# Performance work log

Hardware: AMD Instinct MI355X
Metric: run time of the kernel (lower is better)

The kernel has to match this reference:

```python
import jax, jax.numpy as jnp
import numpy as np

D_MODEL = 4096
HIDDEN = int(8 * D_MODEL / 3)  # 10922, as in the torch __init__
QMAX = 127.0

def fake_quant(t):
    """Symmetric per-tensor int8 fake-quantization (quantize -> dequantize).
    Emulates the quantize/dequantize boundaries of nn.quantized.Linear."""
    s = jnp.maximum(jnp.max(jnp.abs(t)) / QMAX, 1e-8)
    return jnp.clip(jnp.round(t / s), -QMAX, QMAX) * s

def setup_inputs() -> dict:
    key = jax.random.key(0)
    kx, kg, ku, kd, kbg, kbu, kbd = jax.random.split(key, 7)
    x = jax.random.normal(kx, (4096, D_MODEL), dtype=jnp.float32)
    # int8 weights stored dequantized in fp32 (scale * int8 grid applied in fake_quant)
    std = 1.0 / np.sqrt(D_MODEL)
    wg = jax.random.normal(kg, (HIDDEN, D_MODEL), dtype=jnp.float32) * std
    wu = jax.random.normal(ku, (HIDDEN, D_MODEL), dtype=jnp.float32) * std
    wd = jax.random.normal(kd, (D_MODEL, HIDDEN), dtype=jnp.float32) * (1.0 / np.sqrt(HIDDEN))
    bg = jax.random.normal(kbg, (HIDDEN,), dtype=jnp.float32) * 0.01
    bu = jax.random.normal(kbu, (HIDDEN,), dtype=jnp.float32) * 0.01
    bd = jax.random.normal(kbd, (D_MODEL,), dtype=jnp.float32) * 0.01
    return {"x": x, "wg": wg, "wu": wu, "wd": wd, "bg": bg, "bu": bu, "bd": bd}

def reference(x, wg, wu, wd, bg, bu, bd):
    # int8 quantized SwiGLU expert: each nn.quantized.Linear quantizes its
    # input, uses int8 weights, and emits a (re)quantized output.
    xq = fake_quant(x)
    gate = fake_quant(jnp.einsum('td,hd->th', xq, fake_quant(wg)) + bg)
    up = fake_quant(jnp.einsum('td,hd->th', xq, fake_quant(wu)) + bu)
    act = fake_quant(jax.nn.silu(gate) * up)  # SwiGLU, requantized at down_proj input
    out = jnp.einsum('th,dh->td', act, fake_quant(wd)) + bd
    return out
```

## Files before the change

kernel.cpp:

```cpp
#include <hip/hip_runtime.h>

#define D_MODEL 4096
#define HID     10922
#define HIDP    11008
#define MTOK    4096
#define QMAXF   127.0f

typedef _Float16 half8  __attribute__((ext_vector_type(8)));
typedef _Float16 half4v __attribute__((ext_vector_type(4)));
typedef float    floatx4 __attribute__((ext_vector_type(4)));

__device__ __forceinline__ void gl_lds16(const void* g, void* l) {
  __builtin_amdgcn_global_load_lds((__attribute__((address_space(1))) void*)g,
                                   (__attribute__((address_space(3))) void*)l,
                                   16, 0, 0);
}

__device__ __forceinline__ float slot_scale(const unsigned* slots, int idx) {
  return fmaxf(__uint_as_float(slots[idx]) / QMAXF, 1e-8f);
}

__global__ void absmax_k(const float* __restrict__ in, int n4, unsigned* __restrict__ slot) {
  int tid = blockIdx.x * blockDim.x + threadIdx.x;
  int stride = gridDim.x * blockDim.x;
  float m = 0.f;
  const float4* in4 = (const float4*)in;
  for (int i = tid; i < n4; i += stride) {
    float4 v = in4[i];
    m = fmaxf(m, fmaxf(fmaxf(fabsf(v.x), fabsf(v.y)), fmaxf(fabsf(v.z), fabsf(v.w))));
  }
  #pragma unroll
  for (int off = 32; off; off >>= 1) m = fmaxf(m, __shfl_down(m, off));
  __shared__ float sm[4];
  int lane = threadIdx.x & 63, w = threadIdx.x >> 6;
  if (!lane) sm[w] = m;
  __syncthreads();
  if (!threadIdx.x) {
    m = fmaxf(fmaxf(sm[0], sm[1]), fmaxf(sm[2], sm[3]));
    atomicMax(slot, __float_as_uint(m));
  }
}

__global__ void quant_k(const float* __restrict__ in, _Float16* __restrict__ out,
                        int rows_in, int cols_in, int cols_out, int total8,
                        const unsigned* __restrict__ slot) {
  float s = fmaxf(__uint_as_float(*slot) / QMAXF, 1e-8f);
  int t = blockIdx.x * blockDim.x + threadIdx.x;
  if (t >= total8) return;
  int idx = t * 8;
  int r = idx / cols_out;
  int c = idx - r * cols_out;
  half8 h;
  if (r < rows_in && c + 8 <= cols_in) {
    const float2* p = (const float2*)(in + (size_t)r * cols_in + c);
    #pragma unroll
    for (int j = 0; j < 4; ++j) {
      float2 v = p[j];
      float q0 = fminf(fmaxf(rintf(v.x / s), -QMAXF), QMAXF);
      float q1 = fminf(fmaxf(rintf(v.y / s), -QMAXF), QMAXF);
      h[2 * j]     = (_Float16)q0;
      h[2 * j + 1] = (_Float16)q1;
    }
  } else {
    #pragma unroll
    for (int j = 0; j < 8; ++j) {
      int cc = c + j;
      float v = 0.f;
      if (r < rows_in && cc < cols_in) v = in[(size_t)r * cols_in + cc];
      float q = fminf(fmaxf(rintf(v / s), -QMAXF), QMAXF);
      h[j] = (_Float16)q;
    }
  }
  *(half8*)(out + idx) = h;
}

__device__ __forceinline__ float act_val(float g, float u, float sg, float su) {
  float gq = fminf(fmaxf(rintf(g / sg), -QMAXF), QMAXF) * sg;
  float uq = fminf(fmaxf(rintf(u / su), -QMAXF), QMAXF) * su;
  float sig = (gq >= 0.f) ? (1.f / (1.f + expf(-gq)))
                          : (expf(gq) / (1.f + expf(gq)));
  return (gq * sig) * uq;
}

__global__ void act_max_k(const float* __restrict__ gate, const float* __restrict__ up,
                          const unsigned* __restrict__ slots, unsigned* __restrict__ outslot,
                          int n4) {
  float sg = slot_scale(slots, 4);
  float su = slot_scale(slots, 5);
  int tid = blockIdx.x * blockDim.x + threadIdx.x;
  int stride = gridDim.x * blockDim.x;
  float m = 0.f;
  const float4* g4 = (const float4*)gate;
  const float4* u4 = (const float4*)up;
  for (int i = tid; i < n4; i += stride) {
    float4 g = g4[i], u = u4[i];
    m = fmaxf(m, fabsf(act_val(g.x, u.x, sg, su)));
    m = fmaxf(m, fabsf(act_val(g.y, u.y, sg, su)));
    m = fmaxf(m, fabsf(act_val(g.z, u.z, sg, su)));
    m = fmaxf(m, fabsf(act_val(g.w, u.w, sg, su)));
  }
  #pragma unroll
  for (int off = 32; off; off >>= 1) m = fmaxf(m, __shfl_down(m, off));
  __shared__ float sm[4];
  int lane = threadIdx.x & 63, w = threadIdx.x >> 6;
  if (!lane) sm[w] = m;
  __syncthreads();
  if (!threadIdx.x) {
    m = fmaxf(fmaxf(sm[0], sm[1]), fmaxf(sm[2], sm[3]));
    atomicMax(outslot, __float_as_uint(m));
  }
}

__global__ void act_quant_k(const float* __restrict__ gate, const float* __restrict__ up,
                            const unsigned* __restrict__ slots, _Float16* __restrict__ actq,
                            int n4) {
  float sg = slot_scale(slots, 4);
  float su = slot_scale(slots, 5);
  float sa = slot_scale(slots, 6);
  int tid = blockIdx.x * blockDim.x + threadIdx.x;
  int stride = gridDim.x * blockDim.x;
  const float4* g4 = (const float4*)gate;
  const float4* u4 = (const float4*)up;
  for (int i = tid; i < n4; i += stride) {
    float4 g = g4[i], u = u4[i];
    float a0 = act_val(g.x, u.x, sg, su);
    float a1 = act_val(g.y, u.y, sg, su);
    float a2 = act_val(g.z, u.z, sg, su);
    float a3 = act_val(g.w, u.w, sg, su);
    half4v h;
    h[0] = (_Float16)fminf(fmaxf(rintf(a0 / sa), -QMAXF), QMAXF);
    h[1] = (_Float16)fminf(fmaxf(rintf(a1 / sa), -QMAXF), QMAXF);
    h[2] = (_Float16)fminf(fmaxf(rintf(a2 / sa), -QMAXF), QMAXF);
    h[3] = (_Float16)fminf(fmaxf(rintf(a3 / sa), -QMAXF), QMAXF);
    *(half4v*)(actq + (size_t)i * 4) = h;
  }
}

__global__ __launch_bounds__(256) void gemm_k(
    const _Float16* __restrict__ A, const _Float16* __restrict__ B,
    const float* __restrict__ bias, float* __restrict__ C,
    int K, int lda, int ldb, int ldc, int nbias,
    const unsigned* __restrict__ slots, int sa_idx, int sb_idx,
    unsigned* __restrict__ maxslot) {
  __shared__ __align__(16) _Float16 As[128 * 32];
  __shared__ __align__(16) _Float16 Bs[128 * 32];

  const int wave = threadIdx.x >> 6;
  const int lane = threadIdx.x & 63;
  const int wrow = wave >> 1, wcol = wave & 1;
  const int l16 = lane & 15, quad = lane >> 4;
  const int tm = blockIdx.x * 128, tn = blockIdx.y * 128;

  floatx4 acc[4][4] = {};

  const int so = wave * 2048 + lane * 16;
  const char* Ab = (const char*)A;
  const char* Bb = (const char*)B;

  for (int k0 = 0; k0 < K; k0 += 32) {
    #pragma unroll
    for (int p = 0; p < 2; ++p) {
      int bo = so + p * 1024;
      int row = bo >> 6;
      int csrc = ((bo >> 4) & 3) ^ ((row >> 1) & 3);
      gl_lds16(Ab + ((size_t)(tm + row) * lda + k0) * 2 + csrc * 16,
               (char*)As + wave * 2048 + p * 1024);
      gl_lds16(Bb + ((size_t)(tn + row) * ldb + k0) * 2 + csrc * 16,
               (char*)Bs + wave * 2048 + p * 1024);
    }
    __syncthreads();
    half8 af[4], bf[4];
    #pragma unroll
    for (int i = 0; i < 4; ++i) {
      int ra = wrow * 64 + i * 16 + l16;
      int rb = wcol * 64 + i * 16 + l16;
      af[i] = *(const half8*)((const char*)As + (ra * 64 + (quad ^ ((ra >> 1) & 3)) * 16));
      bf[i] = *(const half8*)((const char*)Bs + (rb * 64 + (quad ^ ((rb >> 1) & 3)) * 16));
    }
    #pragma unroll
    for (int i = 0; i < 4; ++i)
      #pragma unroll
      for (int j = 0; j < 4; ++j)
        acc[i][j] = __builtin_amdgcn_mfma_f32_16x16x32_f16(af[i], bf[j], acc[i][j], 0, 0, 0);
    __syncthreads();
  }

  float scale = slot_scale(slots, sa_idx) * slot_scale(slots, sb_idx);
  float mloc = 0.f;
  #pragma unroll
  for (int i = 0; i < 4; ++i) {
    int rg0 = tm + wrow * 64 + i * 16 + quad * 4;
    #pragma unroll
    for (int j = 0; j < 4; ++j) {
      int cg = tn + wcol * 64 + j * 16 + l16;
      float bv = (cg < nbias) ? bias[cg] : 0.f;
      #pragma unroll
      for (int r = 0; r < 4; ++r) {
        float v = acc[i][j][r] * scale + bv;
        C[(size_t)(rg0 + r) * ldc + cg] = v;
        mloc = fmaxf(mloc, fabsf(v));
      }
    }
  }
  #pragma unroll
  for (int off = 32; off; off >>= 1) mloc = fmaxf(mloc, __shfl_down(mloc, off));
  __shared__ float smx[4];
  if (!lane) smx[wave] = mloc;
  __syncthreads();
  if (!threadIdx.x)
    atomicMax(maxslot, __float_as_uint(fmaxf(fmaxf(smx[0], smx[1]), fmaxf(smx[2], smx[3]))));
}

extern "C" void kernel_launch(void* const* d_in, const int* in_sizes, int n_in,
                              void* d_out, int out_size, void* d_ws, size_t ws_size,
                              hipStream_t stream) {
  const float* x  = (const float*)d_in[0];
  const float* wg = (const float*)d_in[1];
  const float* wu = (const float*)d_in[2];
  const float* wd = (const float*)d_in[3];
  const float* bg = (const float*)d_in[4];
  const float* bu = (const float*)d_in[5];
  const float* bd = (const float*)d_in[6];
  float* out = (float*)d_out;

  char* ws = (char*)d_ws;
  unsigned* slots = (unsigned*)ws;
  const size_t XQ_B = (size_t)MTOK * D_MODEL * 2;
  const size_t WQ_B = (size_t)HIDP * D_MODEL * 2;
  const size_t GU_B = (size_t)MTOK * HIDP * 4;

  _Float16* xq   = (_Float16*)(ws + 256);
  _Float16* wgq  = (_Float16*)(ws + 256 + XQ_B);
  _Float16* wuq  = (_Float16*)(ws + 256 + XQ_B + WQ_B);
  float*    gate = (float*)   (ws + 256 + XQ_B + 2 * WQ_B);
  float*    up   = (float*)   (ws + 256 + XQ_B + 2 * WQ_B + GU_B);
  _Float16* actq = wgq;
  _Float16* wdq  = wuq;

  hipMemsetAsync(ws, 0, 256, stream);

  absmax_k<<<2048, 256, 0, stream>>>(x,  MTOK * D_MODEL / 4, slots + 0);
  absmax_k<<<2048, 256, 0, stream>>>(wg, HID * D_MODEL / 4,  slots + 1);
  absmax_k<<<2048, 256, 0, stream>>>(wu, HID * D_MODEL / 4,  slots + 2);
  absmax_k<<<2048, 256, 0, stream>>>(wd, MTOK * HID / 4,     slots + 3);

  {
    int t8 = MTOK * D_MODEL / 8;
    quant_k<<<(t8 + 255) / 256, 256, 0, stream>>>(x, xq, MTOK, D_MODEL, D_MODEL, t8, slots + 0);
    int w8 = HIDP * D_MODEL / 8;
    quant_k<<<(w8 + 255) / 256, 256, 0, stream>>>(wg, wgq, HID, D_MODEL, D_MODEL, w8, slots + 1);
    quant_k<<<(w8 + 255) / 256, 256, 0, stream>>>(wu, wuq, HID, D_MODEL, D_MODEL, w8, slots + 2);
  }

  {
    dim3 g1(MTOK / 128, HIDP / 128);
    gemm_k<<<g1, 256, 0, stream>>>(xq, wgq, bg, gate, D_MODEL, D_MODEL, D_MODEL, HIDP, HID,
                                   slots, 0, 1, slots + 4);
    gemm_k<<<g1, 256, 0, stream>>>(xq, wuq, bu, up,   D_MODEL, D_MODEL, D_MODEL, HIDP, HID,
                                   slots, 0, 2, slots + 5);
  }

  {
    int t8 = MTOK * HIDP / 8;
    quant_k<<<(t8 + 255) / 256, 256, 0, stream>>>(wd, wdq, MTOK, HID, HIDP, t8, slots + 3);
  }

  {
    int n4 = MTOK * HIDP / 4;
    act_max_k<<<4096, 256, 0, stream>>>(gate, up, slots, slots + 6, n4);
    act_quant_k<<<4096, 256, 0, stream>>>(gate, up, slots, actq, n4);
  }

  {
    dim3 g2(MTOK / 128, D_MODEL / 128);
    gemm_k<<<g2, 256, 0, stream>>>(actq, wdq, bd, out, HIDP, HIDP, HIDP, D_MODEL, D_MODEL,
                                   slots, 6, 3, slots + 7);
  }
}
```

Baseline: 2.490 ms.

## Rewrite GEMM as 256x256 tile with double-buffered LDS and phased MFMA pipeline

Replaces the 128x128, BK=32, 4-wave GEMM with a 256x256, BK=64, 8-wave kernel. Global-to-LDS loads are double-buffered and split into per-half stages, so each stage is issued inside one of eight compute phases. Explicit vmcnt waits, scheduling barriers and s_setprio raise around the MFMA bursts overlap memory traffic with matrix math and increase operand reuse per LDS byte. In exchange it uses about 128KB of LDS and large accumulator register state, which likely limits residency to one block per CU. The hand-managed wait counts are fragile.

```diff
diff --git a/kernel.cpp b/kernel.cpp
--- a/kernel.cpp
+++ b/kernel.cpp
@@ -136,63 +136,131 @@
   }
 }
 
-__global__ __launch_bounds__(256) void gemm_k(
+
+#define SBAR() do {                                                           \
+    __builtin_amdgcn_sched_barrier(0);                                        \
+    __builtin_amdgcn_s_barrier();                                             \
+    __builtin_amdgcn_sched_barrier(0);                                        \
+  } while (0)
+
+#define STAGE(GB, LS, LD, TB, KT, BUF, H) do {                                \
+    const char* _s = (GB) + ((size_t)((TB) + (H) * 128 + s_r0) * (LD)         \
+                             + (size_t)(KT) * 64) * 2 + s_cb;                 \
+    char* _d = (char*)(LS) + ((BUF) * 2 + (H)) * 16384 + wave * 1024;         \
+    gl_lds16(_s, _d);                                                         \
+    gl_lds16(_s + (size_t)(LD) * 128, _d + 8192);                             \
+  } while (0)
+
+#define PHASE(BUF, HM, HN, ...) do {                                          \
+    half8 af[4][2], bf[2][2];                                                 \
+    _Pragma("unroll")                                                         \
+    for (int i2 = 0; i2 < 4; ++i2) {                                          \
+      int gr = (HM) * 128 + wrow * 64 + i2 * 16 + l16;                        \
+      const char* pa = (const char*)As + ((BUF) * 2 + (gr >> 7)) * 16384      \
+                       + (gr & 127) * 128;                                    \
+      _Pragma("unroll")                                                       \
+      for (int ks = 0; ks < 2; ++ks)                                          \
+        af[i2][ks] = *(const half8*)(pa + (((ks * 4 + quad) ^ (l16 & 7)) * 16)); \
+    }                                                                         \
+    _Pragma("unroll")                                                         \
+    for (int j2 = 0; j2 < 2; ++j2) {                                          \
+      int gc = (HN) * 128 + wcol * 32 + j2 * 16 + l16;                        \
+      const char* pb = (const char*)Bs + ((BUF) * 2 + (gc >> 7)) * 16384      \
+                       + (gc & 127) * 128;                                    \
+      _Pragma("unroll")                                                       \
+      for (int ks = 0; ks < 2; ++ks)                                          \
+        bf[j2][ks] = *(const half8*)(pb + (((ks * 4 + quad) ^ (l16 & 7)) * 16)); \
+    }                                                                         \
+    __VA_ARGS__;                                                              \
+    SBAR();                                                                   \
+    __builtin_amdgcn_s_setprio(1);                                            \
+    _Pragma("unroll")                                                         \
+    for (int i2 = 0; i2 < 4; ++i2)                                            \
+      _Pragma("unroll")                                                       \
+      for (int j2 = 0; j2 < 2; ++j2)                                          \
+        _Pragma("unroll")                                                     \
+        for (int ks = 0; ks < 2; ++ks)                                        \
+          acc[(HM) * 4 + i2][(HN) * 2 + j2] =                                 \
+              __builtin_amdgcn_mfma_f32_16x16x32_f16(                         \
+                  af[i2][ks], bf[j2][ks],                                     \
+                  acc[(HM) * 4 + i2][(HN) * 2 + j2], 0, 0, 0);                \
+    __builtin_amdgcn_s_setprio(0);                                            \
+    SBAR();                                                                   \
+  } while (0)
+
+__global__ __launch_bounds__(512, 2) void gemm_k(
     const _Float16* __restrict__ A, const _Float16* __restrict__ B,
     const float* __restrict__ bias, float* __restrict__ C,
     int K, int lda, int ldb, int ldc, int nbias,
     const unsigned* __restrict__ slots, int sa_idx, int sb_idx,
     unsigned* __restrict__ maxslot) {
-  __shared__ __align__(16) _Float16 As[128 * 32];
-  __shared__ __align__(16) _Float16 Bs[128 * 32];
-
-  const int wave = threadIdx.x >> 6;
-  const int lane = threadIdx.x & 63;
-  const int wrow = wave >> 1, wcol = wave & 1;
+  __shared__ __align__(16) _Float16 As[2 * 2 * 128 * 64];
+  __shared__ __align__(16) _Float16 Bs[2 * 2 * 128 * 64];
+  __shared__ float smx[8];
+
+  const int tid = threadIdx.x;
+  const int wave = tid >> 6, lane = tid & 63;
+  const int wrow = wave >> 2, wcol = wave & 3;
   const int l16 = lane & 15, quad = lane >> 4;
-  const int tm = blockIdx.x * 128, tn = blockIdx.y * 128;
-
-  floatx4 acc[4][4] = {};
-
-  const int so = wave * 2048 + lane * 16;
+  const int tm = blockIdx.x * 256, tn = blockIdx.y * 256;
+
+  const int s_r0 = wave * 8 + (lane >> 3);
+  const int s_cb = ((lane & 7) ^ (lane >> 3)) * 16;
+
   const char* Ab = (const char*)A;
   const char* Bb = (const char*)B;
 
-  for (int k0 = 0; k0 < K; k0 += 32) {
-    #pragma unroll
-    for (int p = 0; p < 2; ++p) {
-      int bo = so + p * 1024;
-      int row = bo >> 6;
-      int csrc = ((bo >> 4) & 3) ^ ((row >> 1) & 3);
-      gl_lds16(Ab + ((size_t)(tm + row) * lda + k0) * 2 + csrc * 16,
-               (char*)As + wave * 2048 + p * 1024);
-      gl_lds16(Bb + ((size_t)(tn + row) * ldb + k0) * 2 + csrc * 16,
-               (char*)Bs + wave * 2048 + p * 1024);
-    }
-    __syncthreads();
-    half8 af[4], bf[4];
-    #pragma unroll
-    for (int i = 0; i < 4; ++i) {
-      int ra = wrow * 64 + i * 16 + l16;
-      int rb = wcol * 64 + i * 16 + l16;
-      af[i] = *(const half8*)((const char*)As + (ra * 64 + (quad ^ ((ra >> 1) & 3)) * 16));
-      bf[i] = *(const half8*)((const char*)Bs + (rb * 64 + (quad ^ ((rb >> 1) & 3)) * 16));
-    }
-    #pragma unroll
-    for (int i = 0; i < 4; ++i)
-      #pragma unroll
-      for (int j = 0; j < 4; ++j)
-        acc[i][j] = __builtin_amdgcn_mfma_f32_16x16x32_f16(af[i], bf[j], acc[i][j], 0, 0, 0);
-    __syncthreads();
-  }
+  floatx4 acc[8][4] = {};
+
+  const int NT = K >> 6;
+
+  STAGE(Ab, As, lda, tm, 0, 0, 0);
+  STAGE(Ab, As, lda, tm, 0, 0, 1);
+  STAGE(Bb, Bs, ldb, tn, 0, 0, 0);
+  STAGE(Bb, Bs, ldb, tn, 0, 0, 1);
+  STAGE(Ab, As, lda, tm, 1, 1, 0);
+  STAGE(Bb, Bs, ldb, tn, 1, 1, 0);
+  asm volatile("s_waitcnt vmcnt(4)" ::: "memory");
+  SBAR();
+
+  for (int kt = 0; kt + 2 < NT; kt += 2) {
+    PHASE(0, 0, 0, STAGE(Ab, As, lda, tm, kt + 1, 1, 1));
+    PHASE(0, 0, 1, STAGE(Bb, Bs, ldb, tn, kt + 1, 1, 1));
+    PHASE(0, 1, 0, STAGE(Ab, As, lda, tm, kt + 2, 0, 0));
+    PHASE(0, 1, 1, {
+      STAGE(Bb, Bs, ldb, tn, kt + 2, 0, 0);
+      asm volatile("s_waitcnt vmcnt(4)" ::: "memory");
+    });
+    PHASE(1, 0, 0, STAGE(Ab, As, lda, tm, kt + 2, 0, 1));
+    PHASE(1, 0, 1, STAGE(Bb, Bs, ldb, tn, kt + 2, 0, 1));
+    PHASE(1, 1, 0, STAGE(Ab, As, lda, tm, kt + 3, 1, 0));
+    PHASE(1, 1, 1, {
+      STAGE(Bb, Bs, ldb, tn, kt + 3, 1, 0);
+      asm volatile("s_waitcnt vmcnt(4)" ::: "memory");
+    });
+  }
+
+  {
+    const int kt = NT - 2;
+    PHASE(0, 0, 0, STAGE(Ab, As, lda, tm, kt + 1, 1, 1));
+    PHASE(0, 0, 1, STAGE(Bb, Bs, ldb, tn, kt + 1, 1, 1));
+    PHASE(0, 1, 0, );
+    PHASE(0, 1, 1, asm volatile("s_waitcnt vmcnt(0)" ::: "memory"));
+    PHASE(1, 0, 0, );
+    PHASE(1, 0, 1, );
+    PHASE(1, 1, 0, );
+    PHASE(1, 1, 1, );
+  }
+  asm volatile("s_waitcnt vmcnt(0)" ::: "memory");
 
   float scale = slot_scale(slots, sa_idx) * slot_scale(slots, sb_idx);
   float mloc = 0.f;
   #pragma unroll
-  for (int i = 0; i < 4; ++i) {
-    int rg0 = tm + wrow * 64 + i * 16 + quad * 4;
+  for (int i = 0; i < 8; ++i) {
+    int rg0 = tm + (i >> 2) * 128 + wrow * 64 + (i & 3) * 16 + quad * 4;
     #pragma unroll
     for (int j = 0; j < 4; ++j) {
-      int cg = tn + wcol * 64 + j * 16 + l16;
+      int cg = tn + (j >> 1) * 128 + wcol * 32 + (j & 1) * 16 + l16;
       float bv = (cg < nbias) ? bias[cg] : 0.f;
       #pragma unroll
       for (int r = 0; r < 4; ++r) {
@@ -204,11 +272,14 @@
   }
   #pragma unroll
   for (int off = 32; off; off >>= 1) mloc = fmaxf(mloc, __shfl_down(mloc, off));
-  __shared__ float smx[4];
   if (!lane) smx[wave] = mloc;
   __syncthreads();
-  if (!threadIdx.x)
-    atomicMax(maxslot, __float_as_uint(fmaxf(fmaxf(smx[0], smx[1]), fmaxf(smx[2], smx[3]))));
+  if (!tid) {
+    float m = smx[0];
+    #pragma unroll
+    for (int w = 1; w < 8; ++w) m = fmaxf(m, smx[w]);
+    atomicMax(maxslot, __float_as_uint(m));
+  }
 }
 
 extern "C" void kernel_launch(void* const* d_in, const int* in_sizes, int n_in,
@@ -253,10 +324,10 @@
   }
 
   {
-    dim3 g1(MTOK / 128, HIDP / 128);
-    gemm_k<<<g1, 256, 0, stream>>>(xq, wgq, bg, gate, D_MODEL, D_MODEL, D_MODEL, HIDP, HID,
+    dim3 g1(MTOK / 256, HIDP / 256);
+    gemm_k<<<g1, 512, 0, stream>>>(xq, wgq, bg, gate, D_MODEL, D_MODEL, D_MODEL, HIDP, HID,
                                    slots, 0, 1, slots + 4);
-    gemm_k<<<g1, 256, 0, stream>>>(xq, wuq, bu, up,   D_MODEL, D_MODEL, D_MODEL, HIDP, HID,
+    gemm_k<<<g1, 512, 0, stream>>>(xq, wuq, bu, up,   D_MODEL, D_MODEL, D_MODEL, HIDP, HID,
                                    slots, 0, 2, slots + 5);
   }
 
@@ -272,8 +343,8 @@
   }
 
   {
-    dim3 g2(MTOK / 128, D_MODEL / 128);
-    gemm_k<<<g2, 256, 0, stream>>>(actq, wdq, bd, out, HIDP, HIDP, HIDP, D_MODEL, D_MODEL,
+    dim3 g2(MTOK / 256, D_MODEL / 256);
+    gemm_k<<<g2, 512, 0, stream>>>(actq, wdq, bd, out, HIDP, HIDP, HIDP, D_MODEL, D_MODEL,
                                    slots, 6, 3, slots + 7);
   }
 }
```

After: 2.161 ms. -13.2%, faster.
